# Performance work log

Measured on AMD Instinct MI355X. Metric: run time of the kernel, lower is better.

Reference implementation:

```python
import jax, jax.numpy as jnp
import numpy as np

EPS = 1e-15


def _cdist(a, b):
    # batched euclidean pairwise distance, a:[B,N,K] b:[B,M,K] -> [B,N,M]
    d2 = (jnp.sum(a * a, -1)[:, :, None] + jnp.sum(b * b, -1)[:, None, :]
          - 2.0 * jnp.einsum('bik,bjk->bij', a, b))
    return jnp.sqrt(jnp.maximum(d2, 0.0))


def _rank3_diag(d_flat):
    # [B,N] -> [B,N,N] diagonal
    eye = jnp.eye(d_flat.shape[1], dtype=d_flat.dtype)
    return eye * d_flat[:, :, None]


def _trace(m):
    return jnp.einsum('bjj->b', m)


def dense_ct_rewiring(x, adj, s, mask):
    s = jnp.tanh(s)
    m = mask[:, :, None].astype(x.dtype)
    x = x * m
    s = s * m
    k = s.shape[-1]
    d_flat = jnp.sum(adj, axis=-1)              # [B,N]
    d = _rank3_diag(d_flat) + EPS               # EPS added to full matrix (faithful to torch)
    L = d - adj
    out_adj = jnp.einsum('bnk,bnm,bml->bkl', s, L, s)
    ct_num = _trace(out_adj)
    ct_den = _trace(jnp.einsum('bnk,bnm,bml->bkl', s, d, s)) + EPS
    ct_dist = _cdist(s, s)                      # [B,N,N]
    vol = _trace(d)                             # [B]
    ct_dist = ct_dist / vol[:, None, None]
    adj_new = ct_dist * adj
    ct_loss = jnp.mean(ct_num / ct_den)
    ss = jnp.einsum('bnk,bnl->bkl', s, s)
    i_s = jnp.eye(k, dtype=ss.dtype)
    ss_n = jnp.sqrt(jnp.sum(ss * ss, axis=(-1, -2), keepdims=True))
    diff = ss / ss_n - i_s
    ortho_loss = jnp.sqrt(jnp.sum(diff * diff))  # global Frobenius norm, mean of scalar
    return adj_new, ct_loss, ortho_loss


def dense_mincut_pool(x, adj, s, mask):
    s = jax.nn.softmax(s, axis=-1)
    m = mask[:, :, None].astype(x.dtype)
    x = x * m
    s = s * m
    k = s.shape[-1]
    out = jnp.einsum('bnk,bnf->bkf', s, x)
    out_adj = jnp.einsum('bnk,bnm,bml->bkl', s, adj, s)
    mincut_num = _trace(out_adj)
    d_flat = jnp.sum(adj, axis=-1) + EPS
    d = _rank3_diag(d_flat)
    mincut_den = _trace(jnp.einsum('bnk,bnm,bml->bkl', s, d, s))
    mincut_loss = jnp.mean(-(mincut_num / mincut_den))
    ss = jnp.einsum('bnk,bnl->bkl', s, s)
    i_s = jnp.eye(k, dtype=ss.dtype)
    ss_n = jnp.sqrt(jnp.sum(ss * ss, axis=(-1, -2), keepdims=True))
    diff = ss / ss_n - i_s / jnp.sqrt(jnp.asarray(float(k), ss.dtype))
    ortho_loss = jnp.mean(jnp.sqrt(jnp.sum(diff * diff, axis=(-1, -2))))
    # zero diagonal, then symmetric degree normalization
    out_adj = out_adj * (1.0 - i_s)
    dk = jnp.sqrt(jnp.sum(out_adj, axis=-1) + EPS) + EPS  # [B,k]
    out_adj = out_adj / dk[:, None, :] / dk[:, :, None]
    return out, out_adj, mincut_loss, ortho_loss


def dense_graph_conv(x, adj, w_rel, b_rel, w_root):
    # PyG DenseGraphConv(aggr='add'): lin_rel(adj @ x) + lin_root(x)
    return jnp.matmul(jnp.matmul(adj, x), w_rel) + b_rel + jnp.matmul(x, w_root)


def ctnet_forward(x, adj, mask,
                  W_lin1, b_lin1, W_pool1, b_pool1, W_pool2, b_pool2,
                  Wrel1, brel1, Wroot1, Wrel2, brel2, Wroot2,
                  W_lin2, b_lin2, W_lin3, b_lin3):
    x = jnp.matmul(x, W_lin1) + b_lin1
    s1 = jnp.matmul(x, W_pool1) + b_pool1
    adj, ct_loss, ortho1 = dense_ct_rewiring(x, adj, s1, mask)
    x = dense_graph_conv(x, adj, Wrel1, brel1, Wroot1)
    s2 = jnp.matmul(x, W_pool2) + b_pool2
    x, adj, mincut2, ortho2 = dense_mincut_pool(x, adj, s2, mask)
    x = dense_graph_conv(x, adj, Wrel2, brel2, Wroot2)
    x = jnp.sum(x, axis=1)
    x = jax.nn.relu(jnp.matmul(x, W_lin2) + b_lin2)
    x = jnp.matmul(x, W_lin3) + b_lin3
    return jax.nn.log_softmax(x, axis=-1), ct_loss + ortho1, mincut2 + ortho2


def _init_lin(key, fan_in, fan_out):
    k1, k2 = jax.random.split(key)
    lim = 1.0 / np.sqrt(fan_in)
    W = jax.random.uniform(k1, (fan_in, fan_out), jnp.float32, -lim, lim)
    b = jax.random.uniform(k2, (fan_out,), jnp.float32, -lim, lim)
    return W, b


def setup_inputs() -> dict:
    key = jax.random.key(0)
    ks = jax.random.split(key, 12)
    B, N, Fin, H, K, OUT, K2 = 16, 1024, 128, 32, 64, 10, 16
    x = jax.random.normal(ks[0], (B, N, Fin), jnp.float32)
    adj = jax.random.uniform(ks[1], (B, N, N), jnp.float32)
    mask = jnp.ones((B, N), jnp.bool_)
    W_lin1, b_lin1 = _init_lin(ks[2], Fin, H)
    W_pool1, b_pool1 = _init_lin(ks[3], H, K)
    W_pool2, b_pool2 = _init_lin(ks[4], H, K2)
    Wrel1, brel1 = _init_lin(ks[5], H, H)
    Wroot1, _ = _init_lin(ks[6], H, H)
    Wrel2, brel2 = _init_lin(ks[7], H, H)
    Wroot2, _ = _init_lin(ks[8], H, H)
    W_lin2, b_lin2 = _init_lin(ks[9], H, H)
    W_lin3, b_lin3 = _init_lin(ks[10], H, OUT)
    return dict(x=x, adj=adj, mask=mask,
                W_lin1=W_lin1, b_lin1=b_lin1, W_pool1=W_pool1, b_pool1=b_pool1,
                W_pool2=W_pool2, b_pool2=b_pool2,
                Wrel1=Wrel1, brel1=brel1, Wroot1=Wroot1,
                Wrel2=Wrel2, brel2=brel2, Wroot2=Wroot2,
                W_lin2=W_lin2, b_lin2=b_lin2, W_lin3=W_lin3, b_lin3=b_lin3)


def reference(x, adj, mask,
              W_lin1, b_lin1, W_pool1, b_pool1, W_pool2, b_pool2,
              Wrel1, brel1, Wroot1, Wrel2, brel2, Wroot2,
              W_lin2, b_lin2, W_lin3, b_lin3):
    return ctnet_forward(x, adj, mask,
                         W_lin1, b_lin1, W_pool1, b_pool1, W_pool2, b_pool2,
                         Wrel1, brel1, Wroot1, Wrel2, brel2, Wroot2,
                         W_lin2, b_lin2, W_lin3, b_lin3)
```

## Files before the change

kernel.cpp:

```cpp
#include <hip/hip_runtime.h>

typedef unsigned short u16;
typedef unsigned int   u32;
typedef __attribute__((ext_vector_type(8))) short bf16x8;
typedef __attribute__((ext_vector_type(4))) float f32x4;

#define EPSF 1e-15f

__device__ __forceinline__ float* accp(float* xb, int b, int a) {
    return xb + (size_t)(b*1024 + a/14)*128 + 114 + (a % 14);
}

__device__ __forceinline__ float bf2f(u16 u) {
    union { u32 i; float f; } v; v.i = ((u32)u) << 16; return v.f;
}
__device__ __forceinline__ u16 f2bf(float f) {
    union { u32 i; float f; } v; v.f = f;
    u32 r = v.i + 0x7fffu + ((v.i >> 16) & 1u);
    return (u16)(r >> 16);
}

__global__ __launch_bounds__(256) void k_a(float* xb,
        const float* __restrict__ W1, const float* __restrict__ b1,
        const float* __restrict__ Wp1, const float* __restrict__ bp1)
{
    __shared__ float W1s[128*32];
    __shared__ float Wp1s[32*64];
    __shared__ float xs[4][128];
    __shared__ float x1s[4][32];
    int tid = threadIdx.x;
    for (int i = tid; i < 128*32; i += 256) W1s[i] = W1[i];
    for (int i = tid; i < 32*64; i += 256) Wp1s[i] = Wp1[i];
    int w = tid >> 6, l = tid & 63;
    int r = blockIdx.x*4 + w;
    float* xr = xb + (size_t)r*128;
    xs[w][l]      = xr[l];
    xs[w][l + 64] = xr[l + 64];
    __syncthreads();
    if (l < 32) xr[32 + l] = 0.f;
    if (l == 33) xr[96] = 0.f;
    if (l < 15) xr[113 + l] = 0.f;
    if (l < 32) {
        float acc = b1[l];
        for (int f = 0; f < 128; ++f) acc += xs[w][f]*W1s[f*32 + l];
        x1s[w][l] = acc;
    }
    __syncthreads();
    if (l < 32) xr[64 + l] = x1s[w][l];
    {
        float acc = bp1[l];
        for (int h = 0; h < 32; ++h) acc += x1s[w][h]*Wp1s[h*64 + l];
        float sv = tanhf(acc);
        u32 me = (u32)f2bf(sv);
        u32 nb = __shfl_down(me, 1);
        if (!(l & 1)) ((u32*)xr)[l >> 1] = me | (nb << 16);
        float svr = bf2f((u16)me);
        float q = svr*svr;
        for (int off = 32; off; off >>= 1) q += __shfl_down(q, off);
        if (l == 0) xr[112] = q;
    }
}

__global__ __launch_bounds__(256) void k_c(const float* __restrict__ adj, float* xb,
                                           u32* __restrict__ anb)
{
    __shared__ __align__(16) u16 BufA[64*72];
    __shared__ __align__(16) u16 BufB[64*72];
    __shared__ __align__(16) u16 BufX[32*72];
    __shared__ float qAs[64], qBs[64];
    __shared__ float pw[2][4];
    int tid = threadIdx.x;
    int tjq = blockIdx.x, ti = blockIdx.y, b = blockIdx.z;
    const u32* xu = (const u32*)xb;
    for (int e = tid; e < 2048; e += 256) {
        int n = e >> 5, c = e & 31;
        *(u32*)&BufA[n*72 + c*2] = xu[(size_t)(b*1024 + ti*64 + n)*128 + c];
    }
    if (tid < 64) qAs[tid] = xb[(size_t)(b*1024 + ti*64 + tid)*128 + 112];
    int w = tid >> 6, lane = tid & 63;
    int q = lane >> 4, c16 = lane & 15;
    int rloc = w*16 + c16;
    size_t rowg = (size_t)(b*1024 + ti*64 + rloc);
    float4 a4s[2][4];
    #pragma unroll
    for (int t = 0; t < 4; ++t)
        a4s[0][t] = *(const float4*)&adj[rowg*1024 + (tjq*4)*64 + t*16 + q*4];
    __syncthreads();
    bf16x8 bfr0 = *(const bf16x8*)&BufA[rloc*72 + q*8];
    bf16x8 bfr1 = *(const bf16x8*)&BufA[rloc*72 + 32 + q*8];
    float qa = qAs[rloc];
    float dsum = 0.f, rsum = 0.f, Pt = 0.f, Qt = 0.f;
    f32x4 acc2[2] = {{0.f,0.f,0.f,0.f},{0.f,0.f,0.f,0.f}};
    #pragma unroll
    for (int tjj = 0; tjj < 4; ++tjj) {
        int tj = tjq*4 + tjj;
        __syncthreads();
        if (tjj < 3) {
            #pragma unroll
            for (int t = 0; t < 4; ++t)
                a4s[(tjj+1)&1][t] = *(const float4*)&adj[rowg*1024 + (tj+1)*64 + t*16 + q*4];
        }
        for (int e = tid; e < 2048; e += 256) {
            int n = e >> 5, c = e & 31;
            *(u32*)&BufB[n*72 + c*2] = xu[(size_t)(b*1024 + tj*64 + n)*128 + c];
        }
        for (int e = tid; e < 2048; e += 256) {
            int node = e >> 5, h = e & 31;
            BufX[h*72 + node] = f2bf(xb[(size_t)(b*1024 + tj*64 + node)*128 + 64 + h]);
        }
        if (tid < 64) qBs[tid] = xb[(size_t)(b*1024 + tj*64 + tid)*128 + 112];
        __syncthreads();
        f32x4 g[4];
        #pragma unroll
        for (int t = 0; t < 4; ++t) {
            bf16x8 af0 = *(const bf16x8*)&BufB[(t*16 + c16)*72 + q*8];
            bf16x8 af1 = *(const bf16x8*)&BufB[(t*16 + c16)*72 + 32 + q*8];
            f32x4 gg = {0.f, 0.f, 0.f, 0.f};
            gg = __builtin_amdgcn_mfma_f32_16x16x32_bf16(af0, bfr0, gg, 0, 0, 0);
            gg = __builtin_amdgcn_mfma_f32_16x16x32_bf16(af1, bfr1, gg, 0, 0, 0);
            g[t] = gg;
        }
        #pragma unroll
        for (int t = 0; t < 4; ++t) {
            float4 a4 = a4s[tjj&1][t];
            float4 qb4 = *(const float4*)&qBs[t*16 + q*4];
            float av[4] = {a4.x, a4.y, a4.z, a4.w};
            float qb[4] = {qb4.x, qb4.y, qb4.z, qb4.w};
            float o[4];
            #pragma unroll
            for (int rg = 0; rg < 4; ++rg) {
                float d2v = qa + qb[rg] - 2.f*g[t][rg];
                float dist = sqrtf(fmaxf(d2v, 0.f));
                o[rg] = dist * av[rg];
                dsum += av[rg];
                rsum += o[rg];
                Pt += av[rg]*g[t][rg];
                Qt += g[t][rg]*g[t][rg];
            }
            u32 p0 = (u32)f2bf(o[0]) | ((u32)f2bf(o[1]) << 16);
            u32 p1 = (u32)f2bf(o[2]) | ((u32)f2bf(o[3]) << 16);
            int lidx = rloc*72 + t*16 + q*4;
            *(u32*)&BufA[lidx]     = p0;
            *(u32*)&BufA[lidx + 2] = p1;
            *(uint2*)&anb[rowg*512 + tj*32 + t*8 + q*2] = make_uint2(p0, p1);
        }
        __syncthreads();
        bf16x8 ya0 = *(const bf16x8*)&BufA[rloc*72 + q*8];
        bf16x8 ya1 = *(const bf16x8*)&BufA[rloc*72 + 32 + q*8];
        #pragma unroll
        for (int t2 = 0; t2 < 2; ++t2) {
            bf16x8 yb0 = *(const bf16x8*)&BufX[(t2*16 + c16)*72 + q*8];
            bf16x8 yb1 = *(const bf16x8*)&BufX[(t2*16 + c16)*72 + 32 + q*8];
            acc2[t2] = __builtin_amdgcn_mfma_f32_16x16x32_bf16(ya0, yb0, acc2[t2], 0, 0, 0);
            acc2[t2] = __builtin_amdgcn_mfma_f32_16x16x32_bf16(ya1, yb1, acc2[t2], 0, 0, 0);
        }
    }
    rsum += __shfl_xor(rsum, 16); rsum += __shfl_xor(rsum, 32);
    dsum += __shfl_xor(dsum, 16); dsum += __shfl_xor(dsum, 32);
    if (q == 0) {
        atomicAdd(&xb[rowg*128 + 96],  dsum);
        atomicAdd(&xb[rowg*128 + 113], rsum);
    }
    for (int off = 32; off; off >>= 1) { Pt += __shfl_down(Pt, off); Qt += __shfl_down(Qt, off); }
    if (lane == 0) { pw[0][w] = Pt; pw[1][w] = Qt; }
    __syncthreads();
    if (tid == 0) {
        atomicAdd(accp(xb,b,3), pw[0][0]+pw[0][1]+pw[0][2]+pw[0][3]);
        atomicAdd(accp(xb,b,4), pw[1][0]+pw[1][1]+pw[1][2]+pw[1][3]);
    }
    #pragma unroll
    for (int t2 = 0; t2 < 2; ++t2) {
        int h = t2*16 + c16;
        #pragma unroll
        for (int rg = 0; rg < 4; ++rg) {
            int row = ti*64 + w*16 + q*4 + rg;
            atomicAdd(&xb[(size_t)(b*1024 + row)*128 + 32 + h], acc2[t2][rg]);
        }
    }
}

__global__ __launch_bounds__(256) void k_t(float* xb)
{
    __shared__ float ps[3][4];
    int tid = threadIdx.x;
    int r = blockIdx.x*256 + tid;
    int b = r >> 10;
    const float* xr = xb + (size_t)r*128;
    float d = xr[96], qv = xr[112];
    float s0 = d, s1 = d*qv, s2v = qv;
    for (int off = 32; off; off >>= 1) {
        s0 += __shfl_down(s0, off); s1 += __shfl_down(s1, off); s2v += __shfl_down(s2v, off);
    }
    int w = tid >> 6;
    if ((tid & 63) == 0) { ps[0][w] = s0; ps[1][w] = s1; ps[2][w] = s2v; }
    __syncthreads();
    if (tid == 0) {
        atomicAdd(accp(xb,b,0), ps[0][0]+ps[0][1]+ps[0][2]+ps[0][3]);
        atomicAdd(accp(xb,b,1), ps[1][0]+ps[1][1]+ps[1][2]+ps[1][3]);
        atomicAdd(accp(xb,b,2), ps[2][0]+ps[2][1]+ps[2][2]+ps[2][3]);
    }
}

__global__ __launch_bounds__(256) void k_d2(float* xb,
        const float* __restrict__ Wrel1, const float* __restrict__ brel1,
        const float* __restrict__ Wroot1,
        const float* __restrict__ Wp2, const float* __restrict__ bp2)
{
    __shared__ float ys[32*34];
    __shared__ float x1n[32*34];
    __shared__ float x2s[32*34];
    __shared__ float s2s[32*17];
    __shared__ float Wr[1024], Wo[1024], Wp[512];
    int tid = threadIdx.x;
    int tq = blockIdx.x, b = blockIdx.y;
    int rbase = b*1024 + tq*32;
    float invv = 1.f / (*accp(xb,b,0) + 1024.f*EPSF);
    for (int i = tid; i < 1024; i += 256) { Wr[i] = Wrel1[i]; Wo[i] = Wroot1[i]; }
    for (int i = tid; i < 512; i += 256) Wp[i] = Wp2[i];
    for (int e = tid; e < 1024; e += 256) {
        int r = e >> 5, h = e & 31;
        const float* xr = xb + (size_t)(rbase + r)*128;
        ys[r*34 + h]  = xr[32 + h] * invv;
        x1n[r*34 + h] = xr[64 + h];
    }
    __syncthreads();
    {
        int h = tid & 31, tg = tid >> 5;
        float brl = brel1[h];
        #pragma unroll
        for (int i = 0; i < 4; ++i) {
            int r = tg + 8*i;
            float v = brl;
            for (int j = 0; j < 32; ++j)
                v += ys[r*34 + j]*Wr[j*32 + h] + x1n[r*34 + j]*Wo[j*32 + h];
            x2s[r*34 + h] = v;
        }
    }
    __syncthreads();
    if (tid < 64) {
        int r = tid & 31;
        float lg[16];
        float mx = -1e30f;
        #pragma unroll
        for (int k = 0; k < 16; ++k) {
            float v = bp2[k];
            for (int j = 0; j < 32; ++j) v += x2s[r*34 + j]*Wp[j*16 + k];
            lg[k] = v; mx = fmaxf(mx, v);
        }
        float sum = 0.f;
        #pragma unroll
        for (int k = 0; k < 16; ++k) { lg[k] = expf(lg[k] - mx); sum += lg[k]; }
        float inv = 1.f/sum, q2v = 0.f;
        #pragma unroll
        for (int k = 0; k < 16; ++k) {
            float sv = lg[k]*inv;
            s2s[r*17 + k] = sv;
            xb[(size_t)(rbase + r)*128 + 96 + k] = sv;
            q2v += sv*sv;
        }
        float denp = (xb[(size_t)(rbase + r)*128 + 113]*invv + EPSF)*q2v;
        if (tid >= 32) denp = 0.f;
        for (int off = 32; off; off >>= 1) denp += __shfl_down(denp, off);
        if (tid == 0) atomicAdd(accp(xb,b,5), denp);
    }
    __syncthreads();
    {
        int k = tid >> 4, l = tid & 15;
        float s = 0.f;
        for (int r = 0; r < 32; ++r) s += s2s[r*17 + k]*s2s[r*17 + l];
        atomicAdd(accp(xb,b,774 + tid), s);
    }
    for (int e = tid; e < 512; e += 256) {
        int k = e >> 5, h = e & 31;
        float s = 0.f;
        for (int r = 0; r < 32; ++r) s += s2s[r*17 + k]*x2s[r*34 + h];
        atomicAdd(accp(xb,b,6 + k*32 + h), s);
    }
}

__global__ __launch_bounds__(256) void k_e(const u32* __restrict__ anb, float* xb)
{
    __shared__ __align__(16) u16 BufA[64*72];
    __shared__ __align__(16) u16 BufS[16*72];
    __shared__ __align__(16) u16 BufN[16*72];
    __shared__ __align__(16) u16 zT[16*72];
    int tid = threadIdx.x;
    int miq = blockIdx.x, ni = blockIdx.y, b = blockIdx.z;
    for (int e = tid; e < 1024; e += 256) {
        int node = e >> 4, l = e & 15;
        BufN[l*72 + node] = f2bf(xb[(size_t)(b*1024 + ni*64 + node)*128 + 96 + l]);
    }
    int w = tid >> 6, lane = tid & 63;
    int q = lane >> 4, c16 = lane & 15;
    int rloc = w*16 + c16;
    f32x4 zacc = {0.f, 0.f, 0.f, 0.f};
    #pragma unroll
    for (int mii = 0; mii < 2; ++mii) {
        int mi = miq*2 + mii;
        __syncthreads();
        for (int e = tid; e < 2048; e += 256) {
            int n = e >> 5, c = e & 31;
            *(u32*)&BufA[n*72 + c*2] = anb[(size_t)(b*1024 + ni*64 + n)*512 + mi*32 + c];
        }
        for (int e = tid; e < 1024; e += 256) {
            int node = e >> 4, l = e & 15;
            BufS[l*72 + node] = f2bf(xb[(size_t)(b*1024 + mi*64 + node)*128 + 96 + l]);
        }
        __syncthreads();
        bf16x8 ya0 = *(const bf16x8*)&BufA[rloc*72 + q*8];
        bf16x8 ya1 = *(const bf16x8*)&BufA[rloc*72 + 32 + q*8];
        bf16x8 yb0 = *(const bf16x8*)&BufS[c16*72 + q*8];
        bf16x8 yb1 = *(const bf16x8*)&BufS[c16*72 + 32 + q*8];
        zacc = __builtin_amdgcn_mfma_f32_16x16x32_bf16(ya0, yb0, zacc, 0, 0, 0);
        zacc = __builtin_amdgcn_mfma_f32_16x16x32_bf16(ya1, yb1, zacc, 0, 0, 0);
    }
    #pragma unroll
    for (int rg = 0; rg < 4; ++rg)
        zT[c16*72 + w*16 + q*4 + rg] = f2bf(zacc[rg]);
    __syncthreads();
    if (w == 0) {
        bf16x8 af0 = *(const bf16x8*)&BufN[c16*72 + q*8];
        bf16x8 af1 = *(const bf16x8*)&BufN[c16*72 + 32 + q*8];
        bf16x8 bz0 = *(const bf16x8*)&zT[c16*72 + q*8];
        bf16x8 bz1 = *(const bf16x8*)&zT[c16*72 + 32 + q*8];
        f32x4 oamv = {0.f, 0.f, 0.f, 0.f};
        oamv = __builtin_amdgcn_mfma_f32_16x16x32_bf16(af0, bz0, oamv, 0, 0, 0);
        oamv = __builtin_amdgcn_mfma_f32_16x16x32_bf16(af1, bz1, oamv, 0, 0, 0);
        #pragma unroll
        for (int rg = 0; rg < 4; ++rg)
            atomicAdd(accp(xb, b, 518 + (q*4 + rg)*16 + c16), oamv[rg]);
    }
}

__global__ __launch_bounds__(256) void k_f1(float* xb,
        const float* __restrict__ Wrel2, const float* __restrict__ brel2,
        const float* __restrict__ Wroot2,
        const float* __restrict__ W_lin2, const float* __restrict__ b_lin2,
        const float* __restrict__ W_lin3, const float* __restrict__ b_lin3,
        float* __restrict__ outp)
{
    __shared__ float oam_s[256], ssm_s[256], outm_s[512];
    __shared__ float dks[16], csoa[16];
    __shared__ float cs0[32], cs1[32], xsum[32], x5[32], lgs[10];
    __shared__ float red[4];
    int b = blockIdx.x;
    int tid = threadIdx.x;
    float invv = 1.f / (*accp(xb,b,0) + 1024.f*EPSF);
    oam_s[tid] = *accp(xb,b,518 + tid) * invv;
    ssm_s[tid] = *accp(xb,b,774 + tid);
    for (int e = tid; e < 512; e += 256) outm_s[e] = *accp(xb,b,6 + e);
    __syncthreads();
    if (tid < 16) {
        float rsv = 0.f;
        for (int l = 0; l < 16; ++l) if (l != tid) rsv += oam_s[tid*16 + l];
        dks[tid] = sqrtf(fmaxf(rsv, 0.f) + EPSF) + EPSF;
    }
    {
        float v = ssm_s[tid];
        float p = v*v;
        for (int off = 32; off; off >>= 1) p += __shfl_down(p, off);
        if ((tid & 63) == 0) red[tid >> 6] = p;
    }
    __syncthreads();
    if (tid < 16) {
        float s = 0.f;
        for (int k2 = 0; k2 < 16; ++k2)
            if (k2 != tid) s += oam_s[k2*16 + tid] / dks[k2];
        csoa[tid] = s / dks[tid];
    }
    if (tid < 32) {
        float s0 = 0.f, s1 = 0.f;
        for (int l = 0; l < 16; ++l) {
            float ov = outm_s[l*32 + tid];
            s0 += ov;
            s1 += csoa[l] * ov;
        }
        cs0[tid] = s0; cs1[tid] = s1;
    }
    if (tid == 64) {
        float T1v  = *accp(xb,b,1);
        float Pgv  = *accp(xb,b,3);
        float Q2v  = *accp(xb,b,4);
        float Tq1v = *accp(xb,b,2);
        float T2v  = *accp(xb,b,5);
        *accp(xb,b,1030) = (T1v - Pgv) / (T1v + EPSF);
        *accp(xb,b,1031) = 65.f - 2.f*Tq1v/sqrtf(fmaxf(Q2v, 1e-30f));
        float tr2 = 0.f, trs = 0.f;
        for (int k2 = 0; k2 < 16; ++k2) { tr2 += oam_s[k2*17]; trs += ssm_s[k2*17]; }
        *accp(xb,b,1032) = -tr2 / T2v;
        float fr2 = red[0] + red[1] + red[2] + red[3];
        *accp(xb,b,1033) = sqrtf(fmaxf(2.f - trs/(2.f*sqrtf(fmaxf(fr2, 1e-30f))), 0.f));
    }
    __syncthreads();
    if (tid < 32) {
        float v = 16.f * brel2[tid];
        for (int j = 0; j < 32; ++j)
            v += cs1[j]*Wrel2[j*32 + tid] + cs0[j]*Wroot2[j*32 + tid];
        xsum[tid] = v;
    }
    __syncthreads();
    if (tid < 32) {
        float v = b_lin2[tid];
        for (int j = 0; j < 32; ++j) v += xsum[j]*W_lin2[j*32 + tid];
        x5[tid] = fmaxf(v, 0.f);
    }
    __syncthreads();
    if (tid < 10) {
        float v = b_lin3[tid];
        for (int j = 0; j < 32; ++j) v += x5[j]*W_lin3[j*10 + tid];
        lgs[tid] = v;
    }
    __syncthreads();
    if (tid < 10) {
        float mx = -1e30f;
        for (int t = 0; t < 10; ++t) mx = fmaxf(mx, lgs[t]);
        float sum = 0.f;
        for (int t = 0; t < 10; ++t) sum += expf(lgs[t] - mx);
        outp[b*10 + tid] = lgs[tid] - mx - logf(sum);
    }
}

__global__ __launch_bounds__(64) void k_f2(float* xb, float* __restrict__ outp)
{
    int tid = threadIdx.x;
    int b2 = tid & 15, which = tid >> 4;
    float v = *accp(xb, b2, 1030 + which);
    for (int off = 1; off < 16; off <<= 1) v += __shfl_xor(v, off);
    float ct = __shfl(v, 0);
    float o1 = __shfl(v, 16);
    float mc = __shfl(v, 32);
    float o2 = __shfl(v, 48);
    if (tid == 0) {
        outp[160] = ct/16.f + sqrtf(fmaxf(o1, 0.f));
        outp[161] = mc/16.f + o2/16.f;
    }
}

extern "C" void kernel_launch(void* const* d_in, const int* in_sizes, int n_in,
                              void* d_out, int out_size, void* d_ws, size_t ws_size,
                              hipStream_t stream)
{
    float* xb        = (float*)d_in[0];
    const float* adj = (const float*)d_in[1];
    const float* W_lin1 = (const float*)d_in[3];
    const float* b_lin1 = (const float*)d_in[4];
    const float* W_pool1= (const float*)d_in[5];
    const float* b_pool1= (const float*)d_in[6];
    const float* W_pool2= (const float*)d_in[7];
    const float* b_pool2= (const float*)d_in[8];
    const float* Wrel1  = (const float*)d_in[9];
    const float* brel1  = (const float*)d_in[10];
    const float* Wroot1 = (const float*)d_in[11];
    const float* Wrel2  = (const float*)d_in[12];
    const float* brel2  = (const float*)d_in[13];
    const float* Wroot2 = (const float*)d_in[14];
    const float* W_lin2 = (const float*)d_in[15];
    const float* b_lin2 = (const float*)d_in[16];
    const float* W_lin3 = (const float*)d_in[17];
    const float* b_lin3 = (const float*)d_in[18];
    u32* anb = (u32*)d_ws;
    (void)ws_size; (void)in_sizes; (void)n_in; (void)out_size;

    k_a<<<dim3(4096),      dim3(256), 0, stream>>>(xb, W_lin1, b_lin1, W_pool1, b_pool1);
    k_c<<<dim3(4,16,16),   dim3(256), 0, stream>>>(adj, xb, anb);
    k_t<<<dim3(64),        dim3(256), 0, stream>>>(xb);
    k_d2<<<dim3(32,16),    dim3(256), 0, stream>>>(xb, Wrel1, brel1, Wroot1,
                                                   W_pool2, b_pool2);
    k_e<<<dim3(8,16,16),   dim3(256), 0, stream>>>(anb, xb);
    k_f1<<<dim3(16),       dim3(256), 0, stream>>>(xb, Wrel2, brel2, Wroot2,
                                                   W_lin2, b_lin2, W_lin3, b_lin3,
                                                   (float*)d_out);
    k_f2<<<dim3(1),        dim3(64),  0, stream>>>(xb, (float*)d_out);
}
```

Before: 245.9 us.

## Split adjacency-weighted GEMM out of k_c into new k_y kernel, vectorize loads

Moves the second GEMM (new adjacency times x1) out of the distance kernel k_c into a separate k_y kernel that reuses the stored bf16 adjacency with a long K loop. k_c then handles one 64-column tile per block with a 4x larger grid and no inner loop. The k_t reduction is folded into k_y, k_d2 stores the softmax assignments as packed bf16 so k_e can load them directly, and several loaders now use float4 accesses. k_a processes 16 rows per block so the weights are staged in LDS fewer times. The cost is an extra launch and re-reading the anb buffer from global memory.

```diff
diff --git a/kernel.cpp b/kernel.cpp
--- a/kernel.cpp
+++ b/kernel.cpp
@@ -26,134 +26,115 @@
 {
     __shared__ float W1s[128*32];
     __shared__ float Wp1s[32*64];
-    __shared__ float xs[4][128];
-    __shared__ float x1s[4][32];
-    int tid = threadIdx.x;
-    for (int i = tid; i < 128*32; i += 256) W1s[i] = W1[i];
-    for (int i = tid; i < 32*64; i += 256) Wp1s[i] = Wp1[i];
+    __shared__ float xs[16][128];
+    __shared__ float x1s[16][32];
+    int tid = threadIdx.x;
+    for (int i = tid; i < 1024; i += 256)
+        *(float4*)&W1s[i*4] = *(const float4*)&W1[i*4];
+    for (int i = tid; i < 512; i += 256)
+        *(float4*)&Wp1s[i*4] = *(const float4*)&Wp1[i*4];
+    int rbase = blockIdx.x*16;
+    for (int e = tid; e < 512; e += 256) {
+        int rr = e >> 5, c = e & 31;
+        *(float4*)&xs[rr][c*4] = *(const float4*)&xb[(size_t)(rbase + rr)*128 + c*4];
+    }
+    __syncthreads();
     int w = tid >> 6, l = tid & 63;
-    int r = blockIdx.x*4 + w;
-    float* xr = xb + (size_t)r*128;
-    xs[w][l]      = xr[l];
-    xs[w][l + 64] = xr[l + 64];
-    __syncthreads();
-    if (l < 32) xr[32 + l] = 0.f;
-    if (l == 33) xr[96] = 0.f;
-    if (l < 15) xr[113 + l] = 0.f;
-    if (l < 32) {
-        float acc = b1[l];
-        for (int f = 0; f < 128; ++f) acc += xs[w][f]*W1s[f*32 + l];
-        x1s[w][l] = acc;
-    }
-    __syncthreads();
-    if (l < 32) xr[64 + l] = x1s[w][l];
-    {
+    #pragma unroll
+    for (int i = 0; i < 4; ++i) {
+        int rr = w*4 + i;
+        float* xr = xb + (size_t)(rbase + rr)*128;
+        if (l < 32) xr[32 + l] = 0.f;
+        if (l == 33) xr[96] = 0.f;
+        if (l < 15) xr[113 + l] = 0.f;
+        if (l < 32) {
+            float acc = b1[l];
+            for (int f = 0; f < 128; ++f) acc += xs[rr][f]*W1s[f*32 + l];
+            x1s[rr][l] = acc;
+        }
+    }
+    __syncthreads();
+    #pragma unroll
+    for (int i = 0; i < 4; ++i) {
+        int rr = w*4 + i;
+        float* xr = xb + (size_t)(rbase + rr)*128;
+        if (l < 32) xr[64 + l] = x1s[rr][l];
         float acc = bp1[l];
-        for (int h = 0; h < 32; ++h) acc += x1s[w][h]*Wp1s[h*64 + l];
+        for (int h = 0; h < 32; ++h) acc += x1s[rr][h]*Wp1s[h*64 + l];
         float sv = tanhf(acc);
         u32 me = (u32)f2bf(sv);
         u32 nb = __shfl_down(me, 1);
         if (!(l & 1)) ((u32*)xr)[l >> 1] = me | (nb << 16);
         float svr = bf2f((u16)me);
-        float q = svr*svr;
-        for (int off = 32; off; off >>= 1) q += __shfl_down(q, off);
-        if (l == 0) xr[112] = q;
-    }
-}
-
-__global__ __launch_bounds__(256) void k_c(const float* __restrict__ adj, float* xb,
-                                           u32* __restrict__ anb)
+        float qv = svr*svr;
+        for (int off = 32; off; off >>= 1) qv += __shfl_down(qv, off);
+        if (l == 0) xr[112] = qv;
+    }
+}
+
+__global__ __launch_bounds__(256, 6) void k_c(const float* __restrict__ adj, float* xb,
+                                              u32* __restrict__ anb)
 {
     __shared__ __align__(16) u16 BufA[64*72];
     __shared__ __align__(16) u16 BufB[64*72];
-    __shared__ __align__(16) u16 BufX[32*72];
-    __shared__ float qAs[64], qBs[64];
+    __shared__ __align__(16) float qAs[64], qBs[64];
     __shared__ float pw[2][4];
     int tid = threadIdx.x;
-    int tjq = blockIdx.x, ti = blockIdx.y, b = blockIdx.z;
-    const u32* xu = (const u32*)xb;
-    for (int e = tid; e < 2048; e += 256) {
-        int n = e >> 5, c = e & 31;
-        *(u32*)&BufA[n*72 + c*2] = xu[(size_t)(b*1024 + ti*64 + n)*128 + c];
-    }
-    if (tid < 64) qAs[tid] = xb[(size_t)(b*1024 + ti*64 + tid)*128 + 112];
+    int tj = blockIdx.x, ti = blockIdx.y, b = blockIdx.z;
     int w = tid >> 6, lane = tid & 63;
     int q = lane >> 4, c16 = lane & 15;
     int rloc = w*16 + c16;
     size_t rowg = (size_t)(b*1024 + ti*64 + rloc);
-    float4 a4s[2][4];
+    float4 a4s[4];
     #pragma unroll
     for (int t = 0; t < 4; ++t)
-        a4s[0][t] = *(const float4*)&adj[rowg*1024 + (tjq*4)*64 + t*16 + q*4];
+        a4s[t] = *(const float4*)&adj[rowg*1024 + tj*64 + t*16 + q*4];
+    const u32* xu = (const u32*)xb;
+    for (int e = tid; e < 512; e += 256) {
+        int n = e >> 3, c = e & 7;
+        *(float4*)&BufA[n*72 + c*8] = *(const float4*)&xu[(size_t)(b*1024 + ti*64 + n)*128 + c*4];
+    }
+    for (int e = tid; e < 512; e += 256) {
+        int n = e >> 3, c = e & 7;
+        *(float4*)&BufB[n*72 + c*8] = *(const float4*)&xu[(size_t)(b*1024 + tj*64 + n)*128 + c*4];
+    }
+    if (tid < 64) qAs[tid] = xb[(size_t)(b*1024 + ti*64 + tid)*128 + 112];
+    else if (tid < 128) qBs[tid - 64] = xb[(size_t)(b*1024 + tj*64 + (tid - 64))*128 + 112];
     __syncthreads();
     bf16x8 bfr0 = *(const bf16x8*)&BufA[rloc*72 + q*8];
     bf16x8 bfr1 = *(const bf16x8*)&BufA[rloc*72 + 32 + q*8];
     float qa = qAs[rloc];
+    f32x4 g[4];
+    #pragma unroll
+    for (int t = 0; t < 4; ++t) {
+        bf16x8 af0 = *(const bf16x8*)&BufB[(t*16 + c16)*72 + q*8];
+        bf16x8 af1 = *(const bf16x8*)&BufB[(t*16 + c16)*72 + 32 + q*8];
+        f32x4 gg = {0.f, 0.f, 0.f, 0.f};
+        gg = __builtin_amdgcn_mfma_f32_16x16x32_bf16(af0, bfr0, gg, 0, 0, 0);
+        gg = __builtin_amdgcn_mfma_f32_16x16x32_bf16(af1, bfr1, gg, 0, 0, 0);
+        g[t] = gg;
+    }
     float dsum = 0.f, rsum = 0.f, Pt = 0.f, Qt = 0.f;
-    f32x4 acc2[2] = {{0.f,0.f,0.f,0.f},{0.f,0.f,0.f,0.f}};
-    #pragma unroll
-    for (int tjj = 0; tjj < 4; ++tjj) {
-        int tj = tjq*4 + tjj;
-        __syncthreads();
-        if (tjj < 3) {
-            #pragma unroll
-            for (int t = 0; t < 4; ++t)
-                a4s[(tjj+1)&1][t] = *(const float4*)&adj[rowg*1024 + (tj+1)*64 + t*16 + q*4];
-        }
-        for (int e = tid; e < 2048; e += 256) {
-            int n = e >> 5, c = e & 31;
-            *(u32*)&BufB[n*72 + c*2] = xu[(size_t)(b*1024 + tj*64 + n)*128 + c];
-        }
-        for (int e = tid; e < 2048; e += 256) {
-            int node = e >> 5, h = e & 31;
-            BufX[h*72 + node] = f2bf(xb[(size_t)(b*1024 + tj*64 + node)*128 + 64 + h]);
-        }
-        if (tid < 64) qBs[tid] = xb[(size_t)(b*1024 + tj*64 + tid)*128 + 112];
-        __syncthreads();
-        f32x4 g[4];
-        #pragma unroll
-        for (int t = 0; t < 4; ++t) {
-            bf16x8 af0 = *(const bf16x8*)&BufB[(t*16 + c16)*72 + q*8];
-            bf16x8 af1 = *(const bf16x8*)&BufB[(t*16 + c16)*72 + 32 + q*8];
-            f32x4 gg = {0.f, 0.f, 0.f, 0.f};
-            gg = __builtin_amdgcn_mfma_f32_16x16x32_bf16(af0, bfr0, gg, 0, 0, 0);
-            gg = __builtin_amdgcn_mfma_f32_16x16x32_bf16(af1, bfr1, gg, 0, 0, 0);
-            g[t] = gg;
-        }
-        #pragma unroll
-        for (int t = 0; t < 4; ++t) {
-            float4 a4 = a4s[tjj&1][t];
-            float4 qb4 = *(const float4*)&qBs[t*16 + q*4];
-            float av[4] = {a4.x, a4.y, a4.z, a4.w};
-            float qb[4] = {qb4.x, qb4.y, qb4.z, qb4.w};
-            float o[4];
-            #pragma unroll
-            for (int rg = 0; rg < 4; ++rg) {
-                float d2v = qa + qb[rg] - 2.f*g[t][rg];
-                float dist = sqrtf(fmaxf(d2v, 0.f));
-                o[rg] = dist * av[rg];
-                dsum += av[rg];
-                rsum += o[rg];
-                Pt += av[rg]*g[t][rg];
-                Qt += g[t][rg]*g[t][rg];
-            }
-            u32 p0 = (u32)f2bf(o[0]) | ((u32)f2bf(o[1]) << 16);
-            u32 p1 = (u32)f2bf(o[2]) | ((u32)f2bf(o[3]) << 16);
-            int lidx = rloc*72 + t*16 + q*4;
-            *(u32*)&BufA[lidx]     = p0;
-            *(u32*)&BufA[lidx + 2] = p1;
-            *(uint2*)&anb[rowg*512 + tj*32 + t*8 + q*2] = make_uint2(p0, p1);
-        }
-        __syncthreads();
-        bf16x8 ya0 = *(const bf16x8*)&BufA[rloc*72 + q*8];
-        bf16x8 ya1 = *(const bf16x8*)&BufA[rloc*72 + 32 + q*8];
-        #pragma unroll
-        for (int t2 = 0; t2 < 2; ++t2) {
-            bf16x8 yb0 = *(const bf16x8*)&BufX[(t2*16 + c16)*72 + q*8];
-            bf16x8 yb1 = *(const bf16x8*)&BufX[(t2*16 + c16)*72 + 32 + q*8];
-            acc2[t2] = __builtin_amdgcn_mfma_f32_16x16x32_bf16(ya0, yb0, acc2[t2], 0, 0, 0);
-            acc2[t2] = __builtin_amdgcn_mfma_f32_16x16x32_bf16(ya1, yb1, acc2[t2], 0, 0, 0);
-        }
+    #pragma unroll
+    for (int t = 0; t < 4; ++t) {
+        float4 a4 = a4s[t];
+        float4 qb4 = *(const float4*)&qBs[t*16 + q*4];
+        float av[4] = {a4.x, a4.y, a4.z, a4.w};
+        float qb[4] = {qb4.x, qb4.y, qb4.z, qb4.w};
+        float o[4];
+        #pragma unroll
+        for (int rg = 0; rg < 4; ++rg) {
+            float d2v = qa + qb[rg] - 2.f*g[t][rg];
+            float dist = sqrtf(fmaxf(d2v, 0.f));
+            o[rg] = dist * av[rg];
+            dsum += av[rg];
+            rsum += o[rg];
+            Pt += av[rg]*g[t][rg];
+            Qt += g[t][rg]*g[t][rg];
+        }
+        u32 p0 = (u32)f2bf(o[0]) | ((u32)f2bf(o[1]) << 16);
+        u32 p1 = (u32)f2bf(o[2]) | ((u32)f2bf(o[3]) << 16);
+        *(uint2*)&anb[rowg*512 + tj*32 + t*8 + q*2] = make_uint2(p0, p1);
     }
     rsum += __shfl_xor(rsum, 16); rsum += __shfl_xor(rsum, 32);
     dsum += __shfl_xor(dsum, 16); dsum += __shfl_xor(dsum, 32);
@@ -168,36 +149,56 @@
         atomicAdd(accp(xb,b,3), pw[0][0]+pw[0][1]+pw[0][2]+pw[0][3]);
         atomicAdd(accp(xb,b,4), pw[1][0]+pw[1][1]+pw[1][2]+pw[1][3]);
     }
-    #pragma unroll
-    for (int t2 = 0; t2 < 2; ++t2) {
-        int h = t2*16 + c16;
-        #pragma unroll
-        for (int rg = 0; rg < 4; ++rg) {
-            int row = ti*64 + w*16 + q*4 + rg;
-            atomicAdd(&xb[(size_t)(b*1024 + row)*128 + 32 + h], acc2[t2][rg]);
-        }
-    }
-}
-
-__global__ __launch_bounds__(256) void k_t(float* xb)
-{
-    __shared__ float ps[3][4];
-    int tid = threadIdx.x;
-    int r = blockIdx.x*256 + tid;
-    int b = r >> 10;
-    const float* xr = xb + (size_t)r*128;
-    float d = xr[96], qv = xr[112];
-    float s0 = d, s1 = d*qv, s2v = qv;
-    for (int off = 32; off; off >>= 1) {
-        s0 += __shfl_down(s0, off); s1 += __shfl_down(s1, off); s2v += __shfl_down(s2v, off);
-    }
-    int w = tid >> 6;
-    if ((tid & 63) == 0) { ps[0][w] = s0; ps[1][w] = s1; ps[2][w] = s2v; }
-    __syncthreads();
-    if (tid == 0) {
-        atomicAdd(accp(xb,b,0), ps[0][0]+ps[0][1]+ps[0][2]+ps[0][3]);
-        atomicAdd(accp(xb,b,1), ps[1][0]+ps[1][1]+ps[1][2]+ps[1][3]);
-        atomicAdd(accp(xb,b,2), ps[2][0]+ps[2][1]+ps[2][2]+ps[2][3]);
+}
+
+__global__ __launch_bounds__(256) void k_y(const u32* __restrict__ anb, float* xb)
+{
+    __shared__ __align__(16) u16 X[32][264];
+    int tid = threadIdx.x;
+    int kq = blockIdx.x, ni = blockIdx.y, b = blockIdx.z;
+    int w = tid >> 6, lane = tid & 63;
+    int q = lane >> 4, c16 = lane & 15;
+    int rloc = w*16 + c16;
+    size_t rowg = (size_t)(b*1024 + ni*64 + rloc);
+    bf16x8 afv[8];
+    #pragma unroll
+    for (int ks = 0; ks < 8; ++ks)
+        afv[ks] = *(const bf16x8*)&anb[rowg*512 + kq*128 + ks*16 + q*4];
+    for (int e = tid; e < 2048; e += 256) {
+        int m = e >> 3, hq = e & 7;
+        const float4 v = *(const float4*)&xb[(size_t)(b*1024 + kq*256 + m)*128 + 64 + hq*4];
+        X[hq*4 + 0][m] = f2bf(v.x);
+        X[hq*4 + 1][m] = f2bf(v.y);
+        X[hq*4 + 2][m] = f2bf(v.z);
+        X[hq*4 + 3][m] = f2bf(v.w);
+    }
+    __syncthreads();
+    f32x4 acc0 = {0.f,0.f,0.f,0.f}, acc1 = {0.f,0.f,0.f,0.f};
+    #pragma unroll
+    for (int ks = 0; ks < 8; ++ks) {
+        bf16x8 b0 = *(const bf16x8*)&X[c16][ks*32 + q*8];
+        bf16x8 b1v = *(const bf16x8*)&X[c16 + 16][ks*32 + q*8];
+        acc0 = __builtin_amdgcn_mfma_f32_16x16x32_bf16(afv[ks], b0,  acc0, 0, 0, 0);
+        acc1 = __builtin_amdgcn_mfma_f32_16x16x32_bf16(afv[ks], b1v, acc1, 0, 0, 0);
+    }
+    #pragma unroll
+    for (int rg = 0; rg < 4; ++rg) {
+        size_t orow = (size_t)(b*1024 + ni*64 + w*16 + q*4 + rg)*128;
+        atomicAdd(&xb[orow + 32 + c16], acc0[rg]);
+        atomicAdd(&xb[orow + 48 + c16], acc1[rg]);
+    }
+    if (kq == 0 && tid < 64) {
+        const float* xr = xb + (size_t)(b*1024 + ni*64 + tid)*128;
+        float d = xr[96], qv = xr[112];
+        float t0 = d, t1 = d*qv, t2 = qv;
+        for (int off = 32; off; off >>= 1) {
+            t0 += __shfl_down(t0, off); t1 += __shfl_down(t1, off); t2 += __shfl_down(t2, off);
+        }
+        if (tid == 0) {
+            atomicAdd(accp(xb,b,0), t0);
+            atomicAdd(accp(xb,b,1), t1);
+            atomicAdd(accp(xb,b,2), t2);
+        }
     }
 }
 
@@ -251,12 +252,19 @@
         #pragma unroll
         for (int k = 0; k < 16; ++k) { lg[k] = expf(lg[k] - mx); sum += lg[k]; }
         float inv = 1.f/sum, q2v = 0.f;
+        u32 pk[8];
         #pragma unroll
         for (int k = 0; k < 16; ++k) {
             float sv = lg[k]*inv;
             s2s[r*17 + k] = sv;
-            xb[(size_t)(rbase + r)*128 + 96 + k] = sv;
+            u32 bfv = (u32)f2bf(sv);
+            if (k & 1) pk[k>>1] |= bfv << 16; else pk[k>>1] = bfv;
             q2v += sv*sv;
+        }
+        if (tid < 32) {
+            u32* xp = (u32*)(xb + (size_t)(rbase + r)*128);
+            #pragma unroll
+            for (int i2 = 0; i2 < 8; ++i2) xp[i2] = pk[i2];
         }
         float denp = (xb[(size_t)(rbase + r)*128 + 113]*invv + EPSF)*q2v;
         if (tid >= 32) denp = 0.f;
@@ -278,7 +286,7 @@
     }
 }
 
-__global__ __launch_bounds__(256) void k_e(const u32* __restrict__ anb, float* xb)
+__global__ __launch_bounds__(256, 6) void k_e(const u32* __restrict__ anb, float* xb)
 {
     __shared__ __align__(16) u16 BufA[64*72];
     __shared__ __align__(16) u16 BufS[16*72];
@@ -286,9 +294,12 @@
     __shared__ __align__(16) u16 zT[16*72];
     int tid = threadIdx.x;
     int miq = blockIdx.x, ni = blockIdx.y, b = blockIdx.z;
-    for (int e = tid; e < 1024; e += 256) {
-        int node = e >> 4, l = e & 15;
-        BufN[l*72 + node] = f2bf(xb[(size_t)(b*1024 + ni*64 + node)*128 + 96 + l]);
+    const u32* xu = (const u32*)xb;
+    for (int e = tid; e < 512; e += 256) {
+        int node = e >> 3, lw = e & 7;
+        u32 pp = xu[(size_t)(b*1024 + ni*64 + node)*128 + lw];
+        BufN[(lw*2)*72 + node]     = (u16)pp;
+        BufN[(lw*2 + 1)*72 + node] = (u16)(pp >> 16);
     }
     int w = tid >> 6, lane = tid & 63;
     int q = lane >> 4, c16 = lane & 15;
@@ -298,13 +309,16 @@
     for (int mii = 0; mii < 2; ++mii) {
         int mi = miq*2 + mii;
         __syncthreads();
-        for (int e = tid; e < 2048; e += 256) {
-            int n = e >> 5, c = e & 31;
-            *(u32*)&BufA[n*72 + c*2] = anb[(size_t)(b*1024 + ni*64 + n)*512 + mi*32 + c];
-        }
-        for (int e = tid; e < 1024; e += 256) {
-            int node = e >> 4, l = e & 15;
-            BufS[l*72 + node] = f2bf(xb[(size_t)(b*1024 + mi*64 + node)*128 + 96 + l]);
+        for (int e = tid; e < 512; e += 256) {
+            int n = e >> 3, c = e & 7;
+            *(float4*)&BufA[n*72 + c*8] =
+                *(const float4*)&anb[(size_t)(b*1024 + ni*64 + n)*512 + mi*32 + c*4];
+        }
+        for (int e = tid; e < 512; e += 256) {
+            int node = e >> 3, lw = e & 7;
+            u32 pp = xu[(size_t)(b*1024 + mi*64 + node)*128 + lw];
+            BufS[(lw*2)*72 + node]     = (u16)pp;
+            BufS[(lw*2 + 1)*72 + node] = (u16)(pp >> 16);
         }
         __syncthreads();
         bf16x8 ya0 = *(const bf16x8*)&BufA[rloc*72 + q*8];
@@ -461,9 +475,9 @@
     u32* anb = (u32*)d_ws;
     (void)ws_size; (void)in_sizes; (void)n_in; (void)out_size;
 
-    k_a<<<dim3(4096),      dim3(256), 0, stream>>>(xb, W_lin1, b_lin1, W_pool1, b_pool1);
-    k_c<<<dim3(4,16,16),   dim3(256), 0, stream>>>(adj, xb, anb);
-    k_t<<<dim3(64),        dim3(256), 0, stream>>>(xb);
+    k_a<<<dim3(1024),      dim3(256), 0, stream>>>(xb, W_lin1, b_lin1, W_pool1, b_pool1);
+    k_c<<<dim3(16,16,16),  dim3(256), 0, stream>>>(adj, xb, anb);
+    k_y<<<dim3(4,16,16),   dim3(256), 0, stream>>>(anb, xb);
     k_d2<<<dim3(32,16),    dim3(256), 0, stream>>>(xb, Wrel1, brel1, Wroot1,
                                                    W_pool2, b_pool2);
     k_e<<<dim3(8,16,16),   dim3(256), 0, stream>>>(anb, xb);
```

Result: no change. 247.1 us (+0.5%).
